# Optimization experiments

Measured on AMD Instinct MI355X. Metric: run time of the kernel, lower is better.

The kernel has to match this reference:

```python
import jax, jax.numpy as jnp
import numpy as np

B, T, D = 2, 2048, 1024
H = 16
DK = D // H


def setup_inputs() -> dict:
    key = jax.random.key(0)
    ks = jax.random.split(key, 5)
    s = 1.0 / np.sqrt(D)
    return {
        "x": jax.random.normal(ks[0], (B, T, D), dtype=jnp.float32),
        "Wq": jax.random.normal(ks[1], (D, D), dtype=jnp.float32) * s,
        "bq": jnp.zeros((D,), dtype=jnp.float32),
        "Wk": jax.random.normal(ks[2], (D, D), dtype=jnp.float32) * s,
        "bk": jnp.zeros((D,), dtype=jnp.float32),
        "Wv": jax.random.normal(ks[3], (D, D), dtype=jnp.float32) * s,
        "bv": jnp.zeros((D,), dtype=jnp.float32),
        "Wo": jax.random.normal(ks[4], (D, D), dtype=jnp.float32) * s,
        "bo": jnp.zeros((D,), dtype=jnp.float32),
    }


def reference(x, Wq, bq, Wk, bk, Wv, bv, Wo, bo):
    # projections (torch Linear: x @ W.T + b; here W is stored as (in, out))
    Q = x @ Wq + bq  # (B,T,D)
    K = x @ Wk + bk
    V = x @ Wv + bv
    # split heads -> (B,H,T,dk)
    Q = Q.reshape(B, T, H, DK).transpose(0, 2, 1, 3)
    K = K.reshape(B, T, H, DK).transpose(0, 2, 1, 3)
    V = V.reshape(B, T, H, DK).transpose(0, 2, 1, 3)
    scale = 1.0 / jnp.sqrt(jnp.asarray(DK, dtype=x.dtype))
    scores = jnp.einsum("bhqd,bhkd->bhqk", Q, K) * scale  # (B,H,T,T)
    causal = jnp.tril(jnp.ones((T, T), dtype=bool))
    scores = jnp.where(causal, scores, -jnp.inf)
    weights = jax.nn.softmax(scores, axis=-1)
    # dropout is identity in eval mode
    context = jnp.einsum("bhqk,bhkd->bhqd", weights, V)
    context = context.transpose(0, 2, 1, 3).reshape(B, T, D)
    return context @ Wo + bo
```

## Files before the change

### kernel.cpp

```cpp
#include <hip/hip_runtime.h>
#include <hip/hip_bf16.h>

constexpr int Bc = 2;
constexpr int Tc = 2048;
constexpr int Mc = Bc * Tc;
constexpr float CfQ = 0.18033688011112042f;

typedef __attribute__((ext_vector_type(8))) __bf16 bf16x8;
typedef __attribute__((ext_vector_type(4))) __bf16 bf16x4;
typedef __attribute__((ext_vector_type(4))) float floatx4;

__device__ __forceinline__ void gl_lds16(const void* g, void* l) {
    __builtin_amdgcn_global_load_lds(
        (const __attribute__((address_space(1))) void*)g,
        (__attribute__((address_space(3))) void*)l, 16, 0, 0);
}

__global__ __launch_bounds__(256) void prep_all(const float* __restrict__ x,
                                                const float* __restrict__ Wq,
                                                const float* __restrict__ Wk,
                                                const float* __restrict__ Wv,
                                                const float* __restrict__ Wo,
                                                __bf16* __restrict__ xb,
                                                __bf16* __restrict__ Wqkv,
                                                __bf16* __restrict__ Wot) {
    const int z = blockIdx.z;
    const int tid = threadIdx.x;
    if (z >= 4) {
        const int lb = blockIdx.y * 16 + blockIdx.x;
        const size_t base = ((size_t)(z - 4) * 256 + lb) * 4096;
#pragma unroll
        for (int it = 0; it < 4; ++it) {
            const size_t i = base + (size_t)(it * 256 + tid) * 4;
            const float4 v = *(const float4*)(x + i);
            bf16x4 r;
            r[0] = (__bf16)v.x; r[1] = (__bf16)v.y;
            r[2] = (__bf16)v.z; r[3] = (__bf16)v.w;
            *(bf16x4*)(xb + i) = r;
        }
        return;
    }
    __shared__ float t[64][65];
    const float* W = (z == 0) ? Wq : (z == 1) ? Wk : (z == 2) ? Wv : Wo;
    __bf16* Wt = (z < 3) ? Wqkv + (size_t)z * 1024 * 1024 : Wot;
    const int k0 = blockIdx.y * 64, n0 = blockIdx.x * 64;
    const int c = tid & 63, r0 = tid >> 6;
#pragma unroll
    for (int i = 0; i < 16; ++i)
        t[r0 + i * 4][c] = W[(size_t)(k0 + r0 + i * 4) * 1024 + n0 + c];
    __syncthreads();
#pragma unroll
    for (int i = 0; i < 16; ++i) {
        const int r = r0 + i * 4;
        Wt[(size_t)(n0 + r) * 1024 + k0 + c] = (__bf16)t[c][r];
    }
}

template <int TN, bool BF16_OUT, bool FUSE_VT>
__global__ __launch_bounds__(256) void gemm_bt(const __bf16* __restrict__ A,
                                               const __bf16* __restrict__ Bt,
                                               const float* __restrict__ b0,
                                               const float* __restrict__ b1,
                                               const float* __restrict__ b2,
                                               void* __restrict__ Cv,
                                               __bf16* __restrict__ Vt,
                                               int K, int ldc) {
    constexpr int NI = TN / 32;
    __shared__ __bf16 As[128 * 64];
    __shared__ __bf16 Bs[TN * 64];
    const int tid = threadIdx.x, lane = tid & 63, wave = tid >> 6;
    const int wm = wave & 1, wn = wave >> 1;
    const int bm = blockIdx.y * 128, bn = blockIdx.x * TN;
    const __bf16* Ab = A + (size_t)bm * K;
    const __bf16* Bb = Bt + (size_t)bn * K;
    const int quad = lane >> 4, tm = lane & 15;
    const int tsw = tm & 7;

    floatx4 acc[4][NI] = {};

    for (int k0 = 0; k0 < K; k0 += 64) {
#pragma unroll
        for (int i = 0; i < 4; ++i) {
            const int s = i * 256 + tid;
            const int row = s >> 3;
            const int lc = (s & 7) ^ (row & 7);
            gl_lds16(Ab + (size_t)row * K + k0 + lc * 8, As + s * 8);
        }
#pragma unroll
        for (int i = 0; i < TN / 32; ++i) {
            const int s = i * 256 + tid;
            const int row = s >> 3;
            const int lc = (s & 7) ^ (row & 7);
            gl_lds16(Bb + (size_t)row * K + k0 + lc * 8, Bs + s * 8);
        }
        __syncthreads();
        bf16x8 af[4][2], bfv[NI][2];
#pragma unroll
        for (int mi = 0; mi < 4; ++mi) {
            const int row = (wm * 64 + mi * 16 + tm) * 64;
#pragma unroll
            for (int ks = 0; ks < 2; ++ks)
                af[mi][ks] = *(const bf16x8*)(As + row + ((ks * 4 + quad) ^ tsw) * 8);
        }
#pragma unroll
        for (int ni = 0; ni < NI; ++ni) {
            const int row = (wn * (TN / 2) + ni * 16 + tm) * 64;
#pragma unroll
            for (int ks = 0; ks < 2; ++ks)
                bfv[ni][ks] = *(const bf16x8*)(Bs + row + ((ks * 4 + quad) ^ tsw) * 8);
        }
#pragma unroll
        for (int ks = 0; ks < 2; ++ks)
#pragma unroll
            for (int mi = 0; mi < 4; ++mi)
#pragma unroll
                for (int ni = 0; ni < NI; ++ni)
                    acc[mi][ni] = __builtin_amdgcn_mfma_f32_16x16x32_bf16(
                        af[mi][ks], bfv[ni][ks], acc[mi][ni], 0, 0, 0);
        __syncthreads();
    }

#pragma unroll
    for (int ni = 0; ni < NI; ++ni) {
        const int gc = bn + wn * (TN / 2) + ni * 16 + tm;
        const float bias = (gc < 1024) ? b0[gc]
                         : (gc < 2048) ? b1[gc - 1024]
                                       : b2[gc - 2048];
        const float scale = (FUSE_VT && gc < 1024) ? CfQ : 1.0f;
#pragma unroll
        for (int mi = 0; mi < 4; ++mi) {
            const int gr0 = bm + wm * 64 + mi * 16 + quad * 4;
            if (FUSE_VT && gc >= 2048) {
                bf16x4 pv;
#pragma unroll
                for (int r = 0; r < 4; ++r) pv[r] = (__bf16)(acc[mi][ni][r] + bias);
                const int bb = gr0 >> 11, tloc = gr0 & 2047;
                const int hh = (gc - 2048) >> 6, dd = gc & 63;
                const int tperm = (tloc & ~63) + ((tloc >> 2) & 3) * 16 +
                                  ((tloc >> 4) & 3) * 4;
                *(bf16x4*)(Vt + ((size_t)(bb * 16 + hh) * 64 + dd) * 2048 + tperm) = pv;
            } else if (BF16_OUT) {
#pragma unroll
                for (int r = 0; r < 4; ++r)
                    ((__bf16*)Cv)[(size_t)(gr0 + r) * ldc + gc] =
                        (__bf16)((acc[mi][ni][r] + bias) * scale);
            } else {
#pragma unroll
                for (int r = 0; r < 4; ++r)
                    ((float*)Cv)[(size_t)(gr0 + r) * ldc + gc] =
                        acc[mi][ni][r] + bias;
            }
        }
    }
}

__global__ __launch_bounds__(256) void attn_mfma(const __bf16* __restrict__ QK,
                                                 const __bf16* __restrict__ Vt,
                                                 __bf16* __restrict__ ctx) {
    constexpr float NEG = -1e30f;

    __shared__ __bf16 Ks[2][64 * 64];
    __shared__ __bf16 Vts[2][64 * 64];

    const int tid = threadIdx.x, lane = tid & 63, w = tid >> 6;
    const int c = lane & 15, quad = lane >> 4;
    const int bh = blockIdx.y, b = bh >> 4, h = bh & 15;
    const int flip = ((int)blockIdx.x & 1) ^ (((int)blockIdx.y >> 3) & 1);
    const int base = (((int)blockIdx.x >> 1) + ((int)blockIdx.y & 7)) & 15;
    const int qt = flip ? 31 - base : base;
    const int nk = qt + 1;

    const __bf16* Qb = QK + (size_t)(b * Tc) * 2048 + h * 64;
    const __bf16* Kb = Qb + 1024;
    const __bf16* Vtb = Vt + (size_t)bh * 64 * 2048;

    const __bf16* qr = Qb + (size_t)(qt * 64 + w * 16 + c) * 2048;
    const bf16x8 qf0 = *(const bf16x8*)(qr + quad * 8);
    const bf16x8 qf1 = *(const bf16x8*)(qr + 32 + quad * 8);

    float lsum = 0.f;
    floatx4 oa[4] = {};

    const int sw = c & 7;
    int koff0[4], koff1[4];
#pragma unroll
    for (int ni = 0; ni < 4; ++ni) {
        const int krow = ni * 16 + c;
        koff0[ni] = krow * 64 + (quad ^ sw) * 8;
        koff1[ni] = krow * 64 + ((4 + quad) ^ sw) * 8;
    }
    int voff[4][2];
#pragma unroll
    for (int di = 0; di < 4; ++di) {
        const int vrow = di * 16 + c;
#pragma unroll
        for (int pr = 0; pr < 2; ++pr)
            voff[di][pr] = vrow * 64 + ((quad * 2 + pr) ^ sw) * 8;
    }

    const int srow = tid >> 3;
    const int slc = (tid & 7) ^ (srow & 7);
    const __bf16* kg0 = Kb + (size_t)srow * 2048 + slc * 8;
    const __bf16* kg1 = kg0 + (size_t)32 * 2048;
    const __bf16* vg0 = Vtb + (size_t)srow * 2048 + slc * 8;
    const __bf16* vg1 = vg0 + (size_t)32 * 2048;

    gl_lds16(kg0, &Ks[0][tid * 8]);
    gl_lds16(kg1, &Ks[0][tid * 8 + 2048]);
    gl_lds16(vg0, &Vts[0][tid * 8]);
    gl_lds16(vg1, &Vts[0][tid * 8 + 2048]);
    kg0 += (size_t)64 * 2048; kg1 += (size_t)64 * 2048;
    vg0 += 64; vg1 += 64;
    __syncthreads();

    for (int kt = 0; kt < nk; ++kt) {
        const int buf = kt & 1;
        if (kt + 1 < nk) {
            __bf16* kd = &Ks[buf ^ 1][tid * 8];
            __bf16* vd = &Vts[buf ^ 1][tid * 8];
            gl_lds16(kg0, kd);
            gl_lds16(kg1, kd + 2048);
            gl_lds16(vg0, vd);
            gl_lds16(vg1, vd + 2048);
            kg0 += (size_t)64 * 2048; kg1 += (size_t)64 * 2048;
            vg0 += 64; vg1 += 64;
        }
        const __bf16* ks = Ks[buf];
        const __bf16* vs = Vts[buf];

        float sv[4][4];
#pragma unroll
        for (int ni = 0; ni < 4; ++ni) {
            const bf16x8 kb0 = *(const bf16x8*)(ks + koff0[ni]);
            const bf16x8 kb1 = *(const bf16x8*)(ks + koff1[ni]);
            floatx4 a = {};
            a = __builtin_amdgcn_mfma_f32_16x16x32_bf16(kb0, qf0, a, 0, 0, 0);
            a = __builtin_amdgcn_mfma_f32_16x16x32_bf16(kb1, qf1, a, 0, 0, 0);
#pragma unroll
            for (int r = 0; r < 4; ++r) sv[ni][r] = a[r];
        }

        if (kt == qt) {
#pragma unroll
            for (int ni = 0; ni < 4; ++ni)
#pragma unroll
                for (int r = 0; r < 4; ++r)
                    if (ni * 16 + quad * 4 + r > w * 16 + c) sv[ni][r] = NEG;
        }
#pragma unroll
        for (int ni = 0; ni < 4; ++ni)
#pragma unroll
            for (int r = 0; r < 4; ++r) {
                const float p = __builtin_exp2f(sv[ni][r]);
                sv[ni][r] = p;
                lsum += p;
            }

        bf16x8 pb[2];
#pragma unroll
        for (int pr = 0; pr < 2; ++pr)
#pragma unroll
            for (int j = 0; j < 4; ++j) {
                pb[pr][j] = (__bf16)sv[pr * 2][j];
                pb[pr][4 + j] = (__bf16)sv[pr * 2 + 1][j];
            }

#pragma unroll
        for (int di = 0; di < 4; ++di) {
#pragma unroll
            for (int pr = 0; pr < 2; ++pr) {
                const bf16x8 vf = *(const bf16x8*)(vs + voff[di][pr]);
                oa[di] = __builtin_amdgcn_mfma_f32_16x16x32_bf16(
                    vf, pb[pr], oa[di], 0, 0, 0);
            }
        }
        __syncthreads();
    }

    lsum += __shfl_xor(lsum, 16);
    lsum += __shfl_xor(lsum, 32);
    const float inv = 1.f / lsum;
    __bf16* cp = ctx + (size_t)(b * Tc + qt * 64 + w * 16 + c) * 1024 +
                 h * 64 + quad * 4;
#pragma unroll
    for (int di = 0; di < 4; ++di) {
        bf16x4 rv;
#pragma unroll
        for (int r = 0; r < 4; ++r) rv[r] = (__bf16)(oa[di][r] * inv);
        *(bf16x4*)(cp + di * 16) = rv;
    }
}

extern "C" void kernel_launch(void* const* d_in, const int* in_sizes, int n_in,
                              void* d_out, int out_size, void* d_ws, size_t ws_size,
                              hipStream_t stream) {
    const float* x  = (const float*)d_in[0];
    const float* Wq = (const float*)d_in[1];
    const float* bq = (const float*)d_in[2];
    const float* Wk = (const float*)d_in[3];
    const float* bk = (const float*)d_in[4];
    const float* Wv = (const float*)d_in[5];
    const float* bv = (const float*)d_in[6];
    const float* Wo = (const float*)d_in[7];
    const float* bo = (const float*)d_in[8];

    __bf16* xb   = (__bf16*)d_ws;
    __bf16* Wqkv = xb + (size_t)Mc * 1024;
    __bf16* Wot  = Wqkv + (size_t)3072 * 1024;
    __bf16* QKb  = Wot + (size_t)1024 * 1024;
    __bf16* Vtw  = QKb + (size_t)Mc * 2048;
    __bf16* ctxb = xb;

    prep_all<<<dim3(16, 16, 8), 256, 0, stream>>>(x, Wq, Wk, Wv, Wo,
                                                  xb, Wqkv, Wot);

    gemm_bt<128, true, true><<<dim3(24, 32), 256, 0, stream>>>(
        xb, Wqkv, bq, bk, bv, QKb, Vtw, 1024, 2048);

    attn_mfma<<<dim3(32, 32), 256, 0, stream>>>(QKb, Vtw, ctxb);

    gemm_bt<64, false, false><<<dim3(16, 32), 256, 0, stream>>>(
        ctxb, Wot, bo, bo, bo, d_out, nullptr, 1024, 1024);
}
```

Before: 189.2 us.

## Split long causal attention query tiles across two blocks and combine partials

The upper 16 query tiles of each head are split at key tile 16 into two blocks, so per-block work is capped near 16 key tiles instead of up to 32. The grid grows from 1024 to 1536 blocks, evening out the causal load imbalance. A new combine kernel adds the unnormalized bf16 partial outputs and the row sums, then normalizes. The softmax uses no running max, which is what allows plain summation of partials. The cost is an extra launch, workspace traffic for the partials, and extra bf16 rounding of the partial outputs.

```diff
diff --git a/kernel.cpp b/kernel.cpp
--- a/kernel.cpp
+++ b/kernel.cpp
@@ -156,7 +156,9 @@
 
 __global__ __launch_bounds__(256) void attn_mfma(const __bf16* __restrict__ QK,
                                                  const __bf16* __restrict__ Vt,
-                                                 __bf16* __restrict__ ctx) {
+                                                 __bf16* __restrict__ ctx,
+                                                 __bf16* __restrict__ Opart,
+                                                 float* __restrict__ Lpart) {
     constexpr float NEG = -1e30f;
 
     __shared__ __bf16 Ks[2][64 * 64];
@@ -165,10 +167,24 @@
     const int tid = threadIdx.x, lane = tid & 63, w = tid >> 6;
     const int c = lane & 15, quad = lane >> 4;
     const int bh = blockIdx.y, b = bh >> 4, h = bh & 15;
-    const int flip = ((int)blockIdx.x & 1) ^ (((int)blockIdx.y >> 3) & 1);
-    const int base = (((int)blockIdx.x >> 1) + ((int)blockIdx.y & 7)) & 15;
-    const int qt = flip ? 31 - base : base;
-    const int nk = qt + 1;
+    const int x = blockIdx.x;
+
+    int qt, kt0, nv, half;
+    bool split;
+    if (x < 32) {
+        qt = 31 - (x >> 1);
+        half = x & 1;
+        split = true;
+        if (half == 0) { kt0 = 0; nv = 16; }
+        else           { kt0 = 16; nv = qt - 15; }
+    } else {
+        qt = 47 - x;
+        half = 0;
+        split = false;
+        kt0 = 0;
+        nv = qt + 1;
+    }
+    const bool has_diag = (kt0 + nv - 1 == qt);
 
     const __bf16* Qb = QK + (size_t)(b * Tc) * 2048 + h * 64;
     const __bf16* Kb = Qb + 1024;
@@ -200,9 +216,9 @@
 
     const int srow = tid >> 3;
     const int slc = (tid & 7) ^ (srow & 7);
-    const __bf16* kg0 = Kb + (size_t)srow * 2048 + slc * 8;
+    const __bf16* kg0 = Kb + (size_t)(kt0 * 64 + srow) * 2048 + slc * 8;
     const __bf16* kg1 = kg0 + (size_t)32 * 2048;
-    const __bf16* vg0 = Vtb + (size_t)srow * 2048 + slc * 8;
+    const __bf16* vg0 = Vtb + (size_t)srow * 2048 + kt0 * 64 + slc * 8;
     const __bf16* vg1 = vg0 + (size_t)32 * 2048;
 
     gl_lds16(kg0, &Ks[0][tid * 8]);
@@ -213,9 +229,9 @@
     vg0 += 64; vg1 += 64;
     __syncthreads();
 
-    for (int kt = 0; kt < nk; ++kt) {
-        const int buf = kt & 1;
-        if (kt + 1 < nk) {
+    for (int iv = 0; iv < nv; ++iv) {
+        const int buf = iv & 1;
+        if (iv + 1 < nv) {
             __bf16* kd = &Ks[buf ^ 1][tid * 8];
             __bf16* vd = &Vts[buf ^ 1][tid * 8];
             gl_lds16(kg0, kd);
@@ -240,7 +256,7 @@
             for (int r = 0; r < 4; ++r) sv[ni][r] = a[r];
         }
 
-        if (kt == qt) {
+        if (has_diag && iv == nv - 1) {
 #pragma unroll
             for (int ni = 0; ni < 4; ++ni)
 #pragma unroll
@@ -279,15 +295,58 @@
 
     lsum += __shfl_xor(lsum, 16);
     lsum += __shfl_xor(lsum, 32);
-    const float inv = 1.f / lsum;
-    __bf16* cp = ctx + (size_t)(b * Tc + qt * 64 + w * 16 + c) * 1024 +
-                 h * 64 + quad * 4;
-#pragma unroll
-    for (int di = 0; di < 4; ++di) {
-        bf16x4 rv;
-#pragma unroll
-        for (int r = 0; r < 4; ++r) rv[r] = (__bf16)(oa[di][r] * inv);
-        *(bf16x4*)(cp + di * 16) = rv;
+
+    if (split) {
+        const size_t pbase = ((size_t)(bh * 16 + (qt - 16)) * 2 + half);
+        if (quad == 0) Lpart[pbase * 64 + w * 16 + c] = lsum;
+        __bf16* Op = Opart + pbase * 4096 + (size_t)(w * 16 + c) * 64;
+#pragma unroll
+        for (int di = 0; di < 4; ++di) {
+            bf16x4 rv;
+#pragma unroll
+            for (int r = 0; r < 4; ++r) rv[r] = (__bf16)oa[di][r];
+            *(bf16x4*)(Op + di * 16 + quad * 4) = rv;
+        }
+    } else {
+        const float inv = 1.f / lsum;
+        __bf16* cp = ctx + (size_t)(b * Tc + qt * 64 + w * 16 + c) * 1024 +
+                     h * 64 + quad * 4;
+#pragma unroll
+        for (int di = 0; di < 4; ++di) {
+            bf16x4 rv;
+#pragma unroll
+            for (int r = 0; r < 4; ++r) rv[r] = (__bf16)(oa[di][r] * inv);
+            *(bf16x4*)(cp + di * 16) = rv;
+        }
+    }
+}
+
+__global__ __launch_bounds__(256) void attn_combine(const __bf16* __restrict__ Opart,
+                                                    const float* __restrict__ Lpart,
+                                                    __bf16* __restrict__ ctx) {
+    const int tid = threadIdx.x;
+    const int q16 = blockIdx.x, bh = blockIdx.y;
+    const int b = bh >> 4, h = bh & 15;
+    const int qt = q16 + 16;
+    const int q = tid >> 2, ds = (tid & 3) * 16;
+    const size_t pb0 = (size_t)(bh * 16 + q16) * 2;
+    const size_t pb1 = pb0 + 1;
+
+    const float l = Lpart[pb0 * 64 + q] + Lpart[pb1 * 64 + q];
+    const float inv = 1.f / l;
+
+    const __bf16* O0 = Opart + pb0 * 4096 + (size_t)q * 64 + ds;
+    const __bf16* O1 = Opart + pb1 * 4096 + (size_t)q * 64 + ds;
+    __bf16* cp = ctx + (size_t)(b * Tc + qt * 64 + q) * 1024 + h * 64 + ds;
+#pragma unroll
+    for (int u = 0; u < 2; ++u) {
+        const bf16x8 a = *(const bf16x8*)(O0 + u * 8);
+        const bf16x8 bb = *(const bf16x8*)(O1 + u * 8);
+        bf16x8 o;
+#pragma unroll
+        for (int j = 0; j < 8; ++j)
+            o[j] = (__bf16)(((float)a[j] + (float)bb[j]) * inv);
+        *(bf16x8*)(cp + u * 8) = o;
     }
 }
 
@@ -304,12 +363,14 @@
     const float* Wo = (const float*)d_in[7];
     const float* bo = (const float*)d_in[8];
 
-    __bf16* xb   = (__bf16*)d_ws;
-    __bf16* Wqkv = xb + (size_t)Mc * 1024;
-    __bf16* Wot  = Wqkv + (size_t)3072 * 1024;
-    __bf16* QKb  = Wot + (size_t)1024 * 1024;
-    __bf16* Vtw  = QKb + (size_t)Mc * 2048;
-    __bf16* ctxb = xb;
+    __bf16* xb    = (__bf16*)d_ws;
+    __bf16* Wqkv  = xb + (size_t)Mc * 1024;
+    __bf16* Wot   = Wqkv + (size_t)3072 * 1024;
+    __bf16* QKb   = Wot + (size_t)1024 * 1024;
+    __bf16* Vtw   = QKb + (size_t)Mc * 2048;
+    __bf16* Opart = Vtw + (size_t)32 * 64 * 2048;
+    float*  Lpart = (float*)(Opart + (size_t)32 * 16 * 2 * 4096);
+    __bf16* ctxb  = xb;
 
     prep_all<<<dim3(16, 16, 8), 256, 0, stream>>>(x, Wq, Wk, Wv, Wo,
                                                   xb, Wqkv, Wot);
@@ -317,7 +378,8 @@
     gemm_bt<128, true, true><<<dim3(24, 32), 256, 0, stream>>>(
         xb, Wqkv, bq, bk, bv, QKb, Vtw, 1024, 2048);
 
-    attn_mfma<<<dim3(32, 32), 256, 0, stream>>>(QKb, Vtw, ctxb);
+    attn_mfma<<<dim3(48, 32), 256, 0, stream>>>(QKb, Vtw, ctxb, Opart, Lpart);
+    attn_combine<<<dim3(16, 32), 256, 0, stream>>>(Opart, Lpart, ctxb);
 
     gemm_bt<64, false, false><<<dim3(16, 32), 256, 0, stream>>>(
         ctxb, Wot, bo, bo, bo, d_out, nullptr, 1024, 1024);
```

After: 195.5 us. 1.03x slower.
